# Kernel optimization log

Measured on AMD Instinct MI355X. Metric: run time of the kernel, lower is better.

Reference implementation:

```python
import jax, jax.numpy as jnp
import numpy as np

KSIZE = 15
SIGMA = 3.0
PAD = KSIZE // 2


def _gauss_kernel2d():
    g = jnp.arange(KSIZE, dtype=jnp.float32) - KSIZE // 2
    g = jnp.exp(-(g ** 2) / (2.0 * SIGMA * SIGMA))
    g = g / g.sum()
    return g[:, None] * g[None, :]  # [15,15]


def _depthwise_blur(x, k2):
    # x: [B,C,H,W]; 15x15 Gaussian applied per channel (matches per-channel F.conv2d loop)
    C = x.shape[1]
    kernel = jnp.broadcast_to(k2[None, None], (C, 1, KSIZE, KSIZE))
    return jax.lax.conv_general_dilated(
        x, kernel, window_strides=(1, 1), padding=[(PAD, PAD), (PAD, PAD)],
        feature_group_count=C, dimension_numbers=("NCHW", "OIHW", "NCHW"))


def setup_inputs() -> dict:
    key = jax.random.key(0)
    B, C, H, W = 4, 3, 1024, 1024
    x = jax.random.uniform(key, (B, C, H, W), dtype=jnp.float32)
    f32 = lambda v: jnp.asarray(v, dtype=jnp.float32)
    return {
        "x": x,
        "gains": jnp.array([1.1, 1.0, 0.9], dtype=jnp.float32),
        "gamma": f32(0.9),
        "shadow_boost": f32(0.1),
        "highlight_reduce": f32(0.1),
        "brightness": f32(0.05),
        "contrast": f32(1.1),
        "enhance_amount": f32(0.8),
        "softness": f32(0.6),
        "intensity": f32(0.3),
        "rotation": f32(30.0),
        "hardness": f32(2.0),
    }


def reference(x, gains, gamma, shadow_boost, highlight_reduce, brightness,
              contrast, enhance_amount, softness, intensity, rotation, hardness):
    B, C, H, W = x.shape
    k2 = _gauss_kernel2d()

    # WhiteBalanceAdjustment
    x = x * gains.reshape(1, C, 1, 1)
    # ToneCurveAdjustment
    x = jnp.power(x, gamma)
    # ShadowHighlightEnhancement
    hi = jax.nn.sigmoid((x - 0.5) * 10.0)
    x = jnp.clip(x + shadow_boost * (1.0 - hi) - highlight_reduce * hi, 0.0, 1.0)
    # GlobalBrightnessContrastAdjustment
    x = jnp.clip(contrast * (x - 0.5) + 0.5 + brightness, 0.0, 1.0)
    # LocalContrastEnhancement
    local_mean = _depthwise_blur(x, k2)
    x = x + enhance_amount * (x - local_mean)
    # SoftnessFilter
    blurred = _depthwise_blur(x, k2)
    x = softness * blurred + (1.0 - softness) * x
    # GradientNDAdjustment
    ys = jnp.linspace(-1.0, 1.0, H, dtype=jnp.float32)
    xs = jnp.linspace(-1.0, 1.0, W, dtype=jnp.float32)
    grid_y, grid_x = jnp.meshgrid(ys, xs, indexing="ij")
    theta = rotation * (np.pi / 180.0)
    grid_rot = grid_x * jnp.cos(theta) + grid_y * jnp.sin(theta)
    mask = jax.nn.sigmoid(-hardness * grid_rot)[None, None]  # [1,1,H,W]
    x = jnp.clip(x * (1.0 - intensity * mask), 0.0, 1.0)

    return jnp.clip(x, 0.0, 1.0)
```

## Files before the change

kernel.cpp:

```cpp
#include <hip/hip_runtime.h>
#include <math.h>

#define HH 1024
#define WW 1024
#define NPLANES 12
#define PLANE (HH * WW)
#define NTOT (NPLANES * PLANE)

#define TW 64
#define TH 64
#define RH 92
#define RB 78
#define PH 80
#define LDSF (156 * PH)

typedef float vf4 __attribute__((ext_vector_type(4)));

struct W15 { float w[15]; };

__device__ inline float chain1(float t, float gain, float gamma, float sb,
                               float hr, float br, float ct) {
    t = t * gain;
    t = __builtin_amdgcn_exp2f(gamma * __log2f(t));
    float hi = __fdividef(1.0f, 1.0f + __expf((0.5f - t) * 10.0f));
    t = t + sb * (1.0f - hi) - hr * hi;
    t = fminf(fmaxf(t, 0.0f), 1.0f);
    t = ct * (t - 0.5f) + 0.5f + br;
    return fminf(fmaxf(t, 0.0f), 1.0f);
}

__device__ inline int b1r(int r) { return (r < 64) ? (92 + r) : (r + 14); }
__device__ inline int swq(int pr, int q) { return pr * PH + ((q ^ (pr & 3)) << 2); }
__device__ inline int sws(int pr, int j) {
    return pr * PH + ((((j >> 2) ^ (pr & 3)) << 2) | (j & 3));
}

__device__ inline void dot16(const float* f, const W15& wk, float* o) {
#pragma unroll
    for (int j = 0; j < 16; ++j) {
        float a = 0.0f, b = 0.0f;
#pragma unroll
        for (int k = 0; k < 8; ++k)  a += wk.w[k] * f[j + 1 + k];
#pragma unroll
        for (int k = 8; k < 15; ++k) b += wk.w[k] * f[j + 1 + k];
        o[j] = a + b;
    }
}

__device__ inline void tile_map(int& p, int& x0, int& y0, bool& edge) {
    int L = (blockIdx.z * gridDim.y + blockIdx.y) * gridDim.x + blockIdx.x;
    int xcd = L & 7;
    int t   = L >> 3;
    int g   = xcd * 384 + t;
    p = g >> 8;
    int w  = g & 255;
    int ty = w >> 4, tx = w & 15;
    x0 = tx * TW; y0 = ty * TH;
    edge = (tx == 0) || (tx == 15) || (ty == 0) || (ty == 15);
}

__global__ __launch_bounds__(256) void k_point(
    const vf4* __restrict__ x, vf4* __restrict__ o,
    const float* __restrict__ gains,
    const float* __restrict__ pg, const float* __restrict__ psb,
    const float* __restrict__ phr, const float* __restrict__ pbr,
    const float* __restrict__ pct)
{
    int i = blockIdx.x * blockDim.x + threadIdx.x;
    int c = ((i * 8) / PLANE) % 3;
    float gain = gains[c];
    float gamma = *pg, sb = *psb, hr = *phr, br = *pbr, ct = *pct;

    vf4 v0 = __builtin_nontemporal_load(x + 2 * i);
    vf4 v1 = __builtin_nontemporal_load(x + 2 * i + 1);
#pragma unroll
    for (int j = 0; j < 4; ++j) {
        v0[j] = chain1(v0[j], gain, gamma, sb, hr, br, ct);
        v1[j] = chain1(v1[j], gain, gamma, sb, hr, br, ct);
    }
    o[2 * i]     = v0;
    o[2 * i + 1] = v1;
}

__global__ __launch_bounds__(512, 6) void k_fused(
    const float* __restrict__ x1, float* __restrict__ dst,
    const float* __restrict__ penh,
    const float* __restrict__ psoft, const float* __restrict__ pint,
    const float* __restrict__ prot, const float* __restrict__ phard,
    W15 wk)
{
    __shared__ float lds[LDSF];

    int p, x0, y0; bool edge;
    tile_map(p, x0, y0, edge);
    const int tid = threadIdx.x;
    const int tx  = tid & 63;
    const int ty  = tid >> 6;

    const float* __restrict__ plane = x1 + (size_t)p * PLANE;

    if (tid < RH * 5) {
        int r = tid / 5, s = tid - 5 * r;
        int gy  = y0 - 14 + r;
        int gxa = x0 + 16 * s - 16;
        float f[32];
        if (!edge) {
            const float* rp = plane + (size_t)gy * WW + gxa;
#pragma unroll
            for (int i = 0; i < 8; ++i)
                *(float4*)&f[4 * i] = *(const float4*)(rp + 4 * i);
        } else {
            bool rowin = (unsigned)gy < HH;
            const float* rp = plane + (size_t)(rowin ? gy : 0) * WW;
#pragma unroll
            for (int i = 0; i < 8; ++i) {
                int gq = gxa + 4 * i;
                float4 v = make_float4(0.f, 0.f, 0.f, 0.f);
                if (rowin && gq >= 0 && gq + 3 < WW)
                    v = *(const float4*)(rp + gq);
                *(float4*)&f[4 * i] = v;
            }
        }
        float o[16];
        dot16(f, wk, o);
#pragma unroll
        for (int qq = 0; qq < 4; ++qq)
            *(float4*)&lds[swq(r, 4 * s + qq)] = *(float4*)&o[4 * qq];
    }

    float cc[8];
    {
        const float* pc0 = plane + (size_t)(y0 + ty * 8) * WW + (x0 + tx);
#pragma unroll
        for (int jj = 0; jj < 8; ++jj) cc[jj] = pc0[(size_t)jj * WW];
    }
    __syncthreads();

    if (tid < 400) {
        int j = tid % 80, band = tid / 80;
        int rb0 = band * 16;
        int nb  = (band == 4) ? 14 : 16;
        bool xin = (unsigned)(x0 - 8 + j) < WW;
        float win[15];
#pragma unroll
        for (int k = 0; k < 14; ++k) win[k] = lds[sws(rb0 + k, j)];
#pragma unroll
        for (int jj = 0; jj < 16; ++jj) {
            if (jj < nb) {
                win[(jj + 14) % 15] = lds[sws(rb0 + jj + 14, j)];
                float a = 0.0f, b = 0.0f;
#pragma unroll
                for (int k = 0; k < 8; ++k)  a += wk.w[k] * win[(jj + k) % 15];
#pragma unroll
                for (int k = 8; k < 15; ++k) b += wk.w[k] * win[(jj + k) % 15];
                float v = a + b;
                if (edge) {
                    int gy = y0 - 7 + rb0 + jj;
                    if (!((unsigned)gy < HH) || !xin) v = 0.0f;
                }
                lds[sws(b1r(rb0 + jj), j)] = v;
            }
        }
    }
    __syncthreads();

    if (tid < RB * 4) {
        int rb = tid >> 2, s = tid & 3;
        int pb = b1r(rb);
        float f[32];
#pragma unroll
        for (int i = 0; i < 8; ++i)
            *(float4*)&f[4 * i] = *(const float4*)&lds[swq(pb, 4 * s + i)];
        float o[16];
        dot16(f, wk, o);
#pragma unroll
        for (int qq = 0; qq < 4; ++qq)
            *(float4*)&lds[swq(rb, 4 * s + qq)] = *(float4*)&o[4 * qq];
    }
    __syncthreads();

    const float e     = *penh;
    const float sf    = *psoft;
    const float inten = *pint;
    const float hard  = *phard;
    const float theta = (*prot) * 0.017453292519943295f;
    const float cth = __cosf(theta), sth = __sinf(theta);
    const int   gx    = x0 + tx;
    const float gbase = (-1.0f + 2.0f * (float)gx * (1.0f / (float)(WW - 1))) * cth;
    const float ce    = 1.0f + e;

    const float dstep = 2.0f / (float)(HH - 1);
    const float gy0n  = -1.0f + (float)(y0 + ty * 8) * dstep;
    float       E     = __expf(hard * (gbase + gy0n * sth));
    const float q     = __expf(hard * sth * dstep);

    const int ry0 = ty * 8;

    float bb[8];
#pragma unroll
    for (int jj = 0; jj < 8; ++jj)
        bb[jj] = lds[sws(b1r(ry0 + jj + 7), tx + 8)];

    float win[15];
#pragma unroll
    for (int k = 0; k < 14; ++k) win[k] = lds[sws(ry0 + k, tx)];

    float* __restrict__ dstP = dst + (size_t)p * PLANE;
#pragma unroll
    for (int jj = 0; jj < 8; ++jj) {
        win[(jj + 14) % 15] = lds[sws(ry0 + jj + 14, tx)];
        float a = 0.0f, b = 0.0f;
#pragma unroll
        for (int k = 0; k < 8; ++k)  a += wk.w[k] * win[(jj + k) % 15];
#pragma unroll
        for (int k = 8; k < 15; ++k) b += wk.w[k] * win[(jj + k) % 15];
        float B2  = a + b;
        float x2c = ce * cc[jj] - e * bb[jj];
        float bx2 = ce * bb[jj] - e * B2;
        float v   = sf * bx2 + (1.0f - sf) * x2c;
        int   y   = y0 + ry0 + jj;
        float mask = __fdividef(1.0f, 1.0f + E);
        E *= q;
        v = v * (1.0f - inten * mask);
        v = fminf(fmaxf(v, 0.0f), 1.0f);
        __builtin_nontemporal_store(v, &dstP[(size_t)y * WW + gx]);
    }
}

extern "C" void kernel_launch(void* const* d_in, const int* in_sizes, int n_in,
                              void* d_out, int out_size, void* d_ws, size_t ws_size,
                              hipStream_t stream)
{
    const float* x       = (const float*)d_in[0];
    const float* gains   = (const float*)d_in[1];
    const float* p_gamma = (const float*)d_in[2];
    const float* p_sb    = (const float*)d_in[3];
    const float* p_hr    = (const float*)d_in[4];
    const float* p_br    = (const float*)d_in[5];
    const float* p_ct    = (const float*)d_in[6];
    const float* p_enh   = (const float*)d_in[7];
    const float* p_soft  = (const float*)d_in[8];
    const float* p_int   = (const float*)d_in[9];
    const float* p_rot   = (const float*)d_in[10];
    const float* p_hard  = (const float*)d_in[11];

    float* X1 = (float*)d_ws;

    W15 wk;
    {
        double g[15], sum = 0.0;
        for (int i = 0; i < 15; ++i) { double d = (double)(i - 7); g[i] = exp(-d * d / 18.0); sum += g[i]; }
        for (int i = 0; i < 15; ++i) wk.w[i] = (float)(g[i] / sum);
    }

    k_point<<<dim3(NTOT / 8 / 256), dim3(256), 0, stream>>>(
        (const vf4*)x, (vf4*)X1, gains, p_gamma, p_sb, p_hr, p_br, p_ct);

    dim3 grid(WW / TW, HH / TH, NPLANES);
    k_fused<<<grid, dim3(512), 0, stream>>>(
        X1, (float*)d_out, p_enh, p_soft, p_int, p_rot, p_hard, wk);
}
```

Before: 177.0 us.

## Fuse pointwise tone chain into blur kernel via staged LDS halo loads

Removes the separate pointwise kernel and its intermediate workspace round trip. The fused kernel loads raw input tiles in two 46-row halves, applies the tone chain while staging into a dedicated swizzled LDS region, then runs the horizontal blur from LDS. Center pixels are read from LDS instead of global memory. In exchange, the halo pointwise work is recomputed per tile and extra barriers are added.

```diff
diff --git a/kernel.cpp b/kernel.cpp
--- a/kernel.cpp
+++ b/kernel.cpp
@@ -5,16 +5,15 @@
 #define WW 1024
 #define NPLANES 12
 #define PLANE (HH * WW)
-#define NTOT (NPLANES * PLANE)
 
 #define TW 64
 #define TH 64
 #define RH 92
 #define RB 78
 #define PH 80
+#define AOFF 7360
+#define APITCH 96
 #define LDSF (156 * PH)
-
-typedef float vf4 __attribute__((ext_vector_type(4)));
 
 struct W15 { float w[15]; };
 
@@ -33,6 +32,13 @@
 __device__ inline int swq(int pr, int q) { return pr * PH + ((q ^ (pr & 3)) << 2); }
 __device__ inline int sws(int pr, int j) {
     return pr * PH + ((((j >> 2) ^ (pr & 3)) << 2) | (j & 3));
+}
+__device__ inline int aq(int r, int q) {
+    return AOFF + r * APITCH + (((q & 24) | ((q ^ r) & 7)) << 2);
+}
+__device__ inline int as(int r, int c) {
+    int q = c >> 2;
+    return AOFF + r * APITCH + ((((q & 24) | ((q ^ r) & 7)) << 2) | (c & 3));
 }
 
 __device__ inline void dot16(const float* f, const W15& wk, float* o) {
@@ -59,32 +65,65 @@
     edge = (tx == 0) || (tx == 15) || (ty == 0) || (ty == 15);
 }
 
-__global__ __launch_bounds__(256) void k_point(
-    const vf4* __restrict__ x, vf4* __restrict__ o,
+__device__ inline void stage_A(float* lds, const float* __restrict__ plane,
+                               int x0, int gyb, bool edge, int tid,
+                               float gain, float gamma, float sb,
+                               float hr, float br, float ct) {
+#pragma unroll
+    for (int k = 0; k < 2; ++k) {
+        int u = tid + 512 * k;
+        int r = u / 24, q = u - 24 * r;
+        int gy = gyb + r;
+        int gq = x0 - 16 + 4 * q;
+        float4 v = make_float4(0.f, 0.f, 0.f, 0.f);
+        if (!edge || ((unsigned)gy < HH && gq >= 0 && gq + 3 < WW)) {
+            v = *(const float4*)(plane + (size_t)gy * WW + gq);
+            float* pv = (float*)&v;
+#pragma unroll
+            for (int j = 0; j < 4; ++j)
+                pv[j] = chain1(pv[j], gain, gamma, sb, hr, br, ct);
+        }
+        *(float4*)&lds[aq(r, q)] = v;
+    }
+    if (tid < 46 * 24 - 1024) {
+        int u = tid + 1024;
+        int r = u / 24, q = u - 24 * r;
+        int gy = gyb + r;
+        int gq = x0 - 16 + 4 * q;
+        float4 v = make_float4(0.f, 0.f, 0.f, 0.f);
+        if (!edge || ((unsigned)gy < HH && gq >= 0 && gq + 3 < WW)) {
+            v = *(const float4*)(plane + (size_t)gy * WW + gq);
+            float* pv = (float*)&v;
+#pragma unroll
+            for (int j = 0; j < 4; ++j)
+                pv[j] = chain1(pv[j], gain, gamma, sb, hr, br, ct);
+        }
+        *(float4*)&lds[aq(r, q)] = v;
+    }
+}
+
+__device__ inline void hblur_half(float* lds, int hrow0, int tid, const W15& wk) {
+    if (tid < 46 * 5) {
+        int r = tid / 5, s = tid - 5 * r;
+        float f[32];
+#pragma unroll
+        for (int i = 0; i < 8; ++i)
+            *(float4*)&f[4 * i] = *(const float4*)&lds[aq(r, 4 * s + i)];
+        float o[16];
+        dot16(f, wk, o);
+        int hr_ = hrow0 + r;
+#pragma unroll
+        for (int qq = 0; qq < 4; ++qq)
+            *(float4*)&lds[swq(hr_, 4 * s + qq)] = *(float4*)&o[4 * qq];
+    }
+}
+
+__global__ __launch_bounds__(512, 6) void k_fused(
+    const float* __restrict__ x, float* __restrict__ dst,
     const float* __restrict__ gains,
     const float* __restrict__ pg, const float* __restrict__ psb,
     const float* __restrict__ phr, const float* __restrict__ pbr,
-    const float* __restrict__ pct)
-{
-    int i = blockIdx.x * blockDim.x + threadIdx.x;
-    int c = ((i * 8) / PLANE) % 3;
-    float gain = gains[c];
-    float gamma = *pg, sb = *psb, hr = *phr, br = *pbr, ct = *pct;
-
-    vf4 v0 = __builtin_nontemporal_load(x + 2 * i);
-    vf4 v1 = __builtin_nontemporal_load(x + 2 * i + 1);
-#pragma unroll
-    for (int j = 0; j < 4; ++j) {
-        v0[j] = chain1(v0[j], gain, gamma, sb, hr, br, ct);
-        v1[j] = chain1(v1[j], gain, gamma, sb, hr, br, ct);
-    }
-    o[2 * i]     = v0;
-    o[2 * i + 1] = v1;
-}
-
-__global__ __launch_bounds__(512, 6) void k_fused(
-    const float* __restrict__ x1, float* __restrict__ dst,
-    const float* __restrict__ penh,
+    const float* __restrict__ pct, const float* __restrict__ penh,
     const float* __restrict__ psoft, const float* __restrict__ pint,
     const float* __restrict__ prot, const float* __restrict__ phard,
     W15 wk)
@@ -97,42 +136,29 @@
     const int tx  = tid & 63;
     const int ty  = tid >> 6;
 
-    const float* __restrict__ plane = x1 + (size_t)p * PLANE;
-
-    if (tid < RH * 5) {
-        int r = tid / 5, s = tid - 5 * r;
-        int gy  = y0 - 14 + r;
-        int gxa = x0 + 16 * s - 16;
-        float f[32];
-        if (!edge) {
-            const float* rp = plane + (size_t)gy * WW + gxa;
-#pragma unroll
-            for (int i = 0; i < 8; ++i)
-                *(float4*)&f[4 * i] = *(const float4*)(rp + 4 * i);
-        } else {
-            bool rowin = (unsigned)gy < HH;
-            const float* rp = plane + (size_t)(rowin ? gy : 0) * WW;
-#pragma unroll
-            for (int i = 0; i < 8; ++i) {
-                int gq = gxa + 4 * i;
-                float4 v = make_float4(0.f, 0.f, 0.f, 0.f);
-                if (rowin && gq >= 0 && gq + 3 < WW)
-                    v = *(const float4*)(rp + gq);
-                *(float4*)&f[4 * i] = v;
-            }
-        }
-        float o[16];
-        dot16(f, wk, o);
-#pragma unroll
-        for (int qq = 0; qq < 4; ++qq)
-            *(float4*)&lds[swq(r, 4 * s + qq)] = *(float4*)&o[4 * qq];
-    }
+    const float* __restrict__ plane = x + (size_t)p * PLANE;
+    const float gain  = gains[p % 3];
+    const float gamma = *pg, sb = *psb, hrp = *phr, br = *pbr, ct = *pct;
 
     float cc[8];
-    {
-        const float* pc0 = plane + (size_t)(y0 + ty * 8) * WW + (x0 + tx);
-#pragma unroll
-        for (int jj = 0; jj < 8; ++jj) cc[jj] = pc0[(size_t)jj * WW];
+
+    stage_A(lds, plane, x0, y0 - 14, edge, tid, gain, gamma, sb, hrp, br, ct);
+    __syncthreads();
+    hblur_half(lds, 0, tid, wk);
+    if (ty < 4) {
+#pragma unroll
+        for (int jj = 0; jj < 8; ++jj)
+            cc[jj] = lds[as(ty * 8 + jj + 14, tx + 16)];
+    }
+    __syncthreads();
+
+    stage_A(lds, plane, x0, y0 + 32, edge, tid, gain, gamma, sb, hrp, br, ct);
+    __syncthreads();
+    hblur_half(lds, 46, tid, wk);
+    if (ty >= 4) {
+#pragma unroll
+        for (int jj = 0; jj < 8; ++jj)
+            cc[jj] = lds[as(ty * 8 + jj - 32, tx + 16)];
     }
     __syncthreads();
 
@@ -244,8 +270,6 @@
     const float* p_rot   = (const float*)d_in[10];
     const float* p_hard  = (const float*)d_in[11];
 
-    float* X1 = (float*)d_ws;
-
     W15 wk;
     {
         double g[15], sum = 0.0;
@@ -253,10 +277,8 @@
         for (int i = 0; i < 15; ++i) wk.w[i] = (float)(g[i] / sum);
     }
 
-    k_point<<<dim3(NTOT / 8 / 256), dim3(256), 0, stream>>>(
-        (const vf4*)x, (vf4*)X1, gains, p_gamma, p_sb, p_hr, p_br, p_ct);
-
     dim3 grid(WW / TW, HH / TH, NPLANES);
     k_fused<<<grid, dim3(512), 0, stream>>>(
-        X1, (float*)d_out, p_enh, p_soft, p_int, p_rot, p_hard, wk);
-}
+        x, (float*)d_out, gains, p_gamma, p_sb, p_hr, p_br, p_ct,
+        p_enh, p_soft, p_int, p_rot, p_hard, wk);
+}
```

Result: no change. 175.4 us (-0.9%).
